# Kernel optimization log

Hardware: AMD Instinct MI355X
Metric: run time of the kernel (lower is better)

Reference implementation:

```python
import jax, jax.numpy as jnp
import numpy as np

NEG_SLOPE = 0.2


def gat_conv(x, src, dst, W, a_src, a_dst, bias, concat, num_nodes):
    # x: [N, F_in]; W: [F_in, H*C]; a_src/a_dst: [H, C]
    H, C = a_src.shape
    h = (x @ W).reshape(num_nodes, H, C)               # [N,H,C]
    alpha_s = jnp.sum(h * a_src[None], axis=-1)        # [N,H]
    alpha_d = jnp.sum(h * a_dst[None], axis=-1)        # [N,H]
    e = jax.nn.leaky_relu(alpha_s[src] + alpha_d[dst], NEG_SLOPE)  # [E,H]
    m = jax.ops.segment_max(e, dst, num_segments=num_nodes)
    m = jnp.where(jnp.isfinite(m), m, 0.0)
    ex = jnp.exp(e - m[dst])
    denom = jax.ops.segment_sum(ex, dst, num_segments=num_nodes)
    alpha = ex / (denom[dst] + 1e-16)                  # scatter-softmax over dst
    msg = h[src] * alpha[:, :, None]                   # [E,H,C]
    out = jax.ops.segment_sum(msg, dst, num_segments=num_nodes)  # [N,H,C]
    if concat:
        out = out.reshape(num_nodes, H * C)
    else:
        out = out.mean(axis=1)
    return out + bias


def setup_inputs() -> dict:
    key = jax.random.key(0)
    ks = jax.random.split(key, 12)
    N, E = 50000, 800000
    num_concat, F_in, hid, H1, H2, n_cls = 2, 128, 64, 4, 1, 16
    x_list = jax.random.normal(ks[0], (num_concat, N, F_in), dtype=jnp.float32)
    edge_index = jax.random.randint(ks[1], (2, E), 0, N, dtype=jnp.int64)
    s = 0.1
    W1 = jax.random.normal(ks[2], (num_concat, F_in, H1 * hid), dtype=jnp.float32) * s
    att_src1 = jax.random.normal(ks[3], (num_concat, H1, hid), dtype=jnp.float32) * s
    att_dst1 = jax.random.normal(ks[4], (num_concat, H1, hid), dtype=jnp.float32) * s
    bias1 = jnp.zeros((num_concat, H1 * hid), dtype=jnp.float32)
    W2 = jax.random.normal(ks[5], (hid * H1 * num_concat, H2 * n_cls), dtype=jnp.float32) * s
    att_src2 = jax.random.normal(ks[6], (H2, n_cls), dtype=jnp.float32) * s
    att_dst2 = jax.random.normal(ks[7], (H2, n_cls), dtype=jnp.float32) * s
    bias2 = jnp.zeros((n_cls,), dtype=jnp.float32)
    return {"x_list": x_list, "edge_index": edge_index,
            "W1": W1, "att_src1": att_src1, "att_dst1": att_dst1, "bias1": bias1,
            "W2": W2, "att_src2": att_src2, "att_dst2": att_dst2, "bias2": bias2}


def reference(x_list, edge_index, W1, att_src1, att_dst1, bias1, W2, att_src2, att_dst2, bias2):
    num_concat, N, _ = x_list.shape
    loop = jnp.arange(N, dtype=edge_index.dtype)
    src = jnp.concatenate([edge_index[0], loop])  # PyG add_self_loops=True
    dst = jnp.concatenate([edge_index[1], loop])
    hidden = [jax.nn.elu(gat_conv(x_list[k], src, dst, W1[k], att_src1[k], att_dst1[k],
                                  bias1[k], True, N))
              for k in range(num_concat)]
    x = jnp.concatenate(hidden, axis=-1)           # [N, hid*H1*num_concat]
    out = gat_conv(x, src, dst, W2, att_src2, att_dst2, bias2, False, N)
    return out
```

## Files before the change

### kernel.cpp

```cpp
#include <hip/hip_runtime.h>

#define LEAKY(v) ((v) >= 0.0f ? (v) : 0.2f * (v))

typedef __attribute__((ext_vector_type(8))) short bf16x8;
typedef __attribute__((ext_vector_type(4))) float f32x4;

__device__ __forceinline__ unsigned short f2bf(float f) {
    unsigned int u = __float_as_uint(f);
    unsigned int r = u + 0x7FFFu + ((u >> 16) & 1u);
    return (unsigned short)(r >> 16);
}
__device__ __forceinline__ unsigned int pk2(float a, float b) {
    return (unsigned int)f2bf(a) | ((unsigned int)f2bf(b) << 16);
}
__device__ __forceinline__ float lo16(unsigned int u) { return __uint_as_float(u << 16); }
__device__ __forceinline__ float hi16(unsigned int u) { return __uint_as_float(u & 0xFFFF0000u); }


__global__ __launch_bounds__(256) void count_deg(const int* ei, int* deg, int E, int Etot) {
    int i = blockIdx.x * 256 + threadIdx.x;
    if (i >= Etot) return;
    int d = (i < E) ? ei[E + i] : (i - E);
    atomicAdd(&deg[d], 1);
}

__global__ __launch_bounds__(512) void scan_block(const int* deg, int* excl, int* bsum, int n) {
    __shared__ int s[512];
    int t = threadIdx.x;
    int i = blockIdx.x * 512 + t;
    int v = (i < n) ? deg[i] : 0;
    s[t] = v;
    __syncthreads();
    for (int d = 1; d < 512; d <<= 1) {
        int x = 0;
        if (t >= d) x = s[t - d];
        __syncthreads();
        if (t >= d) s[t] += x;
        __syncthreads();
    }
    if (i < n) excl[i] = s[t] - v;
    if (t == 511) bsum[blockIdx.x] = s[511];
}

__global__ __launch_bounds__(512) void scan_sums(const int* bsum, int* boff, int nb) {
    __shared__ int s[512];
    int t = threadIdx.x;
    int v = (t < nb) ? bsum[t] : 0;
    s[t] = v;
    __syncthreads();
    for (int d = 1; d < 512; d <<= 1) {
        int x = 0;
        if (t >= d) x = s[t - d];
        __syncthreads();
        if (t >= d) s[t] += x;
        __syncthreads();
    }
    boff[t] = s[t] - v;
}

__global__ __launch_bounds__(256) void finalize_off(int* csr, int* cursor, const int* boff, int n, int etot) {
    int i = blockIdx.x * 256 + threadIdx.x;
    if (i < n) {
        int v = csr[i] + boff[i >> 9];
        csr[i] = v;
        cursor[i] = v;
    }
    if (i == 0) csr[n] = etot;
}

__global__ __launch_bounds__(256) void scatter_edge(const int* ei, int* cursor, int* srcs, int* dsts,
                                                    int E, int Etot) {
    int i = blockIdx.x * 256 + threadIdx.x;
    if (i >= Etot) return;
    int s, d;
    if (i < E) { s = ei[i]; d = ei[E + i]; }
    else       { s = i - E; d = s; }
    int pos = atomicAdd(&cursor[d], 1);
    srcs[pos] = s;
    dsts[pos] = d;
}


__global__ __launch_bounds__(256) void wpack(const float* __restrict__ W1, unsigned short* __restrict__ wt1,
                                             const float* __restrict__ W2, unsigned short* __restrict__ wt2) {
    int id = blockIdx.x * 256 + threadIdx.x;
    if (id < 8192) {
        int conv = id >> 12, rem = id & 4095;
        int c = rem >> 4, q = rem & 15;
        const float* src = W1 + (size_t)conv * 32768 + (size_t)(q * 8) * 256 + c;
        float w[8];
#pragma unroll
        for (int j = 0; j < 8; ++j) w[j] = src[j * 256];
        uint4 v;
        v.x = pk2(w[0], w[1]); v.y = pk2(w[2], w[3]);
        v.z = pk2(w[4], w[5]); v.w = pk2(w[6], w[7]);
        *(uint4*)(wt1 + (size_t)conv * 32768 + c * 128 + ((q ^ (c & 7)) << 3)) = v;
    } else if (id < 9216) {
        int id2 = id - 8192;
        int s = id2 >> 6, l = id2 & 63;
        const float* src = W2 + (size_t)(s * 32 + (l >> 4) * 8) * 16 + (l & 15);
        float w[8];
#pragma unroll
        for (int j = 0; j < 8; ++j) w[j] = src[j * 16];
        uint4 v;
        v.x = pk2(w[0], w[1]); v.y = pk2(w[2], w[3]);
        v.z = pk2(w[4], w[5]); v.w = pk2(w[6], w[7]);
        *(uint4*)(wt2 + (size_t)id2 * 8) = v;
    }
}


__global__ __launch_bounds__(256) void gemm1_mfma(const float* __restrict__ x_list,
                                                  const unsigned short* __restrict__ wt1,
                                                  const float* __restrict__ asw, const float* __restrict__ adw,
                                                  unsigned short* __restrict__ hp,
                                                  float* __restrict__ aad, int N) {
    __shared__ unsigned short As[64 * 128];
    __shared__ unsigned short Ws[256 * 128];
    int conv = blockIdx.y;
    int t = threadIdx.x;
    int w = t >> 6, l = t & 63;

    const float* xg = x_list + (size_t)conv * N * 128;
#pragma unroll
    for (int p = 0; p < 4; ++p) {
        int id = p * 256 + t;
        int row = id >> 4, q = id & 15;
        int grow = blockIdx.x * 64 + row;
        uint4 v = make_uint4(0, 0, 0, 0);
        if (grow < N) {
            const float* src = xg + (size_t)grow * 128 + q * 8;
            float4 a = *(const float4*)src;
            float4 b = *(const float4*)(src + 4);
            v.x = pk2(a.x, a.y); v.y = pk2(a.z, a.w);
            v.z = pk2(b.x, b.y); v.w = pk2(b.z, b.w);
        }
        *(uint4*)(As + row * 128 + ((q ^ (row & 7)) << 3)) = v;
    }
    const uint4* wsrc = (const uint4*)(wt1 + (size_t)conv * 32768);
#pragma unroll
    for (int p = 0; p < 16; ++p) {
        int id = p * 256 + t;
        *(uint4*)(Ws + (size_t)id * 8) = wsrc[id];
    }
    __syncthreads();

    f32x4 acc[4][4];
#pragma unroll
    for (int mt = 0; mt < 4; ++mt)
#pragma unroll
        for (int nt = 0; nt < 4; ++nt) acc[mt][nt] = (f32x4){0.f, 0.f, 0.f, 0.f};

    int lr = l & 15, lg = l >> 4;
#pragma unroll
    for (int s = 0; s < 4; ++s) {
        int kq = s * 4 + lg;
        bf16x8 af[4], bf[4];
#pragma unroll
        for (int mt = 0; mt < 4; ++mt) {
            int r = mt * 16 + lr;
            af[mt] = *(const bf16x8*)(As + r * 128 + ((kq ^ (r & 7)) << 3));
        }
#pragma unroll
        for (int nt = 0; nt < 4; ++nt) {
            int c = w * 64 + nt * 16 + lr;
            bf[nt] = *(const bf16x8*)(Ws + c * 128 + ((kq ^ (c & 7)) << 3));
        }
#pragma unroll
        for (int mt = 0; mt < 4; ++mt)
#pragma unroll
            for (int nt = 0; nt < 4; ++nt)
                acc[mt][nt] = __builtin_amdgcn_mfma_f32_16x16x32_bf16(bf[nt], af[mt], acc[mt][nt], 0, 0, 0);
    }

    float4 aswv[4], adwv[4];
#pragma unroll
    for (int nt = 0; nt < 4; ++nt) {
        aswv[nt] = *(const float4*)(asw + conv * 256 + w * 64 + nt * 16 + lg * 4);
        adwv[nt] = *(const float4*)(adw + conv * 256 + w * 64 + nt * 16 + lg * 4);
    }
#pragma unroll
    for (int mt = 0; mt < 4; ++mt) {
        int grow = blockIdx.x * 64 + mt * 16 + lr;
        bool ok = grow < N;
        float sv = 0.f, dv = 0.f;
#pragma unroll
        for (int nt = 0; nt < 4; ++nt) {
            f32x4 a = acc[mt][nt];
            if (ok) {
                uint2 pk;
                pk.x = pk2(a[0], a[1]);
                pk.y = pk2(a[2], a[3]);
                *(uint2*)(hp + (size_t)grow * 512 + conv * 256 + w * 64 + nt * 16 + lg * 4) = pk;
            }
            sv += a[0] * aswv[nt].x + a[1] * aswv[nt].y + a[2] * aswv[nt].z + a[3] * aswv[nt].w;
            dv += a[0] * adwv[nt].x + a[1] * adwv[nt].y + a[2] * adwv[nt].z + a[3] * adwv[nt].w;
        }
        sv += __shfl_xor(sv, 16); sv += __shfl_xor(sv, 32);
        dv += __shfl_xor(dv, 16); dv += __shfl_xor(dv, 32);
        if (l < 16 && ok) {
            aad[(size_t)grow * 16 + conv * 4 + w]     = sv;
            aad[(size_t)grow * 16 + 8 + conv * 4 + w] = dv;
        }
    }
}


__global__ __launch_bounds__(256) void edge_w1(const int* __restrict__ srcs, const int* __restrict__ dsts,
                                               const float* __restrict__ aad,
                                               float* __restrict__ pw, int Etot) {
    int e = blockIdx.x * 256 + threadIdx.x;
    if (e >= Etot) return;
    int s = srcs[e], d = dsts[e];
    float4 as_lo = *(const float4*)(aad + (size_t)s * 16);
    float4 as_hi = *(const float4*)(aad + (size_t)s * 16 + 4);
    float4 ad_lo = *(const float4*)(aad + (size_t)d * 16 + 8);
    float4 ad_hi = *(const float4*)(aad + (size_t)d * 16 + 12);
    float4 p0, p1;
    p0.x = __expf(LEAKY(as_lo.x + ad_lo.x));
    p0.y = __expf(LEAKY(as_lo.y + ad_lo.y));
    p0.z = __expf(LEAKY(as_lo.z + ad_lo.z));
    p0.w = __expf(LEAKY(as_lo.w + ad_lo.w));
    p1.x = __expf(LEAKY(as_hi.x + ad_hi.x));
    p1.y = __expf(LEAKY(as_hi.y + ad_hi.y));
    p1.z = __expf(LEAKY(as_hi.z + ad_hi.z));
    p1.w = __expf(LEAKY(as_hi.w + ad_hi.w));
    *(float4*)(pw + (size_t)e * 8)     = p0;
    *(float4*)(pw + (size_t)e * 8 + 4) = p1;
}


__global__ __launch_bounds__(256) void agg1_both(const unsigned short* __restrict__ hp,
                                                 const float* __restrict__ pw,
                                                 const int* __restrict__ off, const int* __restrict__ srcs,
                                                 const float* __restrict__ b1,
                                                 unsigned short* __restrict__ x2, int N) {
    int n = blockIdx.x * 4 + (threadIdx.x >> 6);
    int lane = threadIdx.x & 63;
    if (n >= N) return;
    int r0 = off[n], r1 = off[n + 1];
    int ch = lane >> 3;

    float acc[8] = {0.f, 0.f, 0.f, 0.f, 0.f, 0.f, 0.f, 0.f};
    float den = 0.f;

    for (int base = r0; base < r1; base += 64) {
        int cnt = min(64, r1 - base);
        int my = (base + lane < r1) ? srcs[base + lane] : 0;
        int j = 0;
        for (; j + 2 <= cnt; j += 2) {
            int s0 = __shfl(my, j);
            int s1 = __shfl(my, j + 1);
            uint4 g0 = *(const uint4*)(hp + (size_t)s0 * 512 + lane * 8);
            uint4 g1 = *(const uint4*)(hp + (size_t)s1 * 512 + lane * 8);
            float p0 = pw[(size_t)(base + j) * 8 + ch];
            float p1 = pw[(size_t)(base + j + 1) * 8 + ch];
            den += p0; den += p1;
            acc[0] += p0 * lo16(g0.x); acc[1] += p0 * hi16(g0.x);
            acc[2] += p0 * lo16(g0.y); acc[3] += p0 * hi16(g0.y);
            acc[4] += p0 * lo16(g0.z); acc[5] += p0 * hi16(g0.z);
            acc[6] += p0 * lo16(g0.w); acc[7] += p0 * hi16(g0.w);
            acc[0] += p1 * lo16(g1.x); acc[1] += p1 * hi16(g1.x);
            acc[2] += p1 * lo16(g1.y); acc[3] += p1 * hi16(g1.y);
            acc[4] += p1 * lo16(g1.z); acc[5] += p1 * hi16(g1.z);
            acc[6] += p1 * lo16(g1.w); acc[7] += p1 * hi16(g1.w);
        }
        if (j < cnt) {
            int s0 = __shfl(my, j);
            uint4 g0 = *(const uint4*)(hp + (size_t)s0 * 512 + lane * 8);
            float p0 = pw[(size_t)(base + j) * 8 + ch];
            den += p0;
            acc[0] += p0 * lo16(g0.x); acc[1] += p0 * hi16(g0.x);
            acc[2] += p0 * lo16(g0.y); acc[3] += p0 * hi16(g0.y);
            acc[4] += p0 * lo16(g0.z); acc[5] += p0 * hi16(g0.z);
            acc[6] += p0 * lo16(g0.w); acc[7] += p0 * hi16(g0.w);
        }
    }

    float inv = 1.f / (den + 1e-16f);
    const float* bp = b1 + lane * 8;
    unsigned int ow[4];
#pragma unroll
    for (int q = 0; q < 4; ++q) {
        float o0 = acc[q * 2 + 0] * inv + bp[q * 2 + 0];
        float o1 = acc[q * 2 + 1] * inv + bp[q * 2 + 1];
        o0 = o0 > 0.f ? o0 : (__expf(o0) - 1.0f);
        o1 = o1 > 0.f ? o1 : (__expf(o1) - 1.0f);
        ow[q] = pk2(o0, o1);
    }
    uint4 ov = make_uint4(ow[0], ow[1], ow[2], ow[3]);
    *(uint4*)(x2 + (size_t)n * 512 + lane * 8) = ov;
}


__global__ __launch_bounds__(256) void gemm2_mfma(const unsigned short* __restrict__ x2,
                                                  const unsigned short* __restrict__ wt2,
                                                  const float* __restrict__ asw2, const float* __restrict__ adw2,
                                                  float* __restrict__ h2,
                                                  float* __restrict__ as2, float* __restrict__ ad2, int N) {
    int t = threadIdx.x;
    int w = t >> 6, l = t & 63;
    int rowbase = (blockIdx.x * 4 + w) * 16;
    if (rowbase >= N) return;
    int lr = l & 15, lg = l >> 4;

    f32x4 acc = (f32x4){0.f, 0.f, 0.f, 0.f};
    const unsigned short* ap = x2 + (size_t)(rowbase + lr) * 512 + lg * 8;
#pragma unroll
    for (int s = 0; s < 16; ++s) {
        bf16x8 av = *(const bf16x8*)(ap + s * 32);
        bf16x8 bv = *(const bf16x8*)(wt2 + ((size_t)s * 64 + l) * 8);
        acc = __builtin_amdgcn_mfma_f32_16x16x32_bf16(av, bv, acc, 0, 0, 0);
    }

    float asv = asw2[lr], adv = adw2[lr];
#pragma unroll
    for (int i = 0; i < 4; ++i) {
        int row = rowbase + lg * 4 + i;
        if (row < N) h2[(size_t)row * 16 + lr] = acc[i];
        float sv = acc[i] * asv, dv = acc[i] * adv;
#pragma unroll
        for (int o = 1; o < 16; o <<= 1) {
            sv += __shfl_xor(sv, o);
            dv += __shfl_xor(dv, o);
        }
        if (lr == 0 && row < N) { as2[row] = sv; ad2[row] = dv; }
    }
}


__global__ __launch_bounds__(256) void agg2(const float* __restrict__ h2,
                                            const float* __restrict__ as2, const float* __restrict__ ad2,
                                            const int* __restrict__ off, const int* __restrict__ srcs,
                                            const float* __restrict__ bias2, float* __restrict__ out, int N) {
    int n = blockIdx.x * 4 + (threadIdx.x >> 6);
    int lane = threadIdx.x & 63;
    if (n >= N) return;
    int r0 = off[n], r1 = off[n + 1];
    float adn = ad2[n];
    int cg = lane & 3, eo = lane >> 2;

    float4 acc = make_float4(0.f, 0.f, 0.f, 0.f);
    float den = 0.f;
    for (int base = r0; base + eo < r1; base += 16) {
        int e = base + eo;
        int s = srcs[e];
        float p = __expf(LEAKY(as2[s] + adn));
        float4 hv = *(const float4*)(h2 + (size_t)s * 16 + cg * 4);
        den += p;
        acc.x += p * hv.x; acc.y += p * hv.y;
        acc.z += p * hv.z; acc.w += p * hv.w;
    }
#pragma unroll
    for (int o = 4; o < 64; o <<= 1) {
        acc.x += __shfl_xor(acc.x, o);
        acc.y += __shfl_xor(acc.y, o);
        acc.z += __shfl_xor(acc.z, o);
        acc.w += __shfl_xor(acc.w, o);
        den   += __shfl_xor(den, o);
    }
    if (eo == 0) {
        float inv = 1.f / (den + 1e-16f);
        float4 b = *(const float4*)(bias2 + cg * 4);
        float4 o4;
        o4.x = acc.x * inv + b.x;
        o4.y = acc.y * inv + b.y;
        o4.z = acc.z * inv + b.z;
        o4.w = acc.w * inv + b.w;
        *(float4*)(out + (size_t)n * 16 + cg * 4) = o4;
    }
}


extern "C" void kernel_launch(void* const* d_in, const int* in_sizes, int n_in,
                              void* d_out, int out_size, void* d_ws, size_t ws_size,
                              hipStream_t stream) {
    const float* x_list = (const float*)d_in[0];
    const int*   ei     = (const int*)d_in[1];
    const float* W1     = (const float*)d_in[2];
    const float* as1w   = (const float*)d_in[3];
    const float* ad1w   = (const float*)d_in[4];
    const float* b1     = (const float*)d_in[5];
    const float* W2     = (const float*)d_in[6];
    const float* as2w   = (const float*)d_in[7];
    const float* ad2w   = (const float*)d_in[8];
    const float* b2     = (const float*)d_in[9];
    float* out = (float*)d_out;

    const int N = in_sizes[0] / 256;
    const int E = in_sizes[1] / 2;
    const int Etot = E + N;

    char* ws = (char*)d_ws;
    size_t woff = 0;
    auto alloc = [&](size_t bytes) {
        char* p = ws + woff;
        woff = (woff + bytes + 255) & ~(size_t)255;
        return p;
    };
    int*   csr    = (int*)alloc((size_t)(N + 1) * 4);
    int*   cursor = (int*)alloc((size_t)N * 4);
    int*   srcs   = (int*)alloc((size_t)Etot * 4);
    int*   dsts   = (int*)alloc((size_t)Etot * 4);
    int*   bsum   = (int*)alloc(512 * 4);
    int*   boff   = (int*)alloc(512 * 4);
    float* aad    = (float*)alloc((size_t)N * 16 * 4);
    float* as2    = (float*)alloc((size_t)N * 4);
    float* ad2    = (float*)alloc((size_t)N * 4);
    unsigned short* wt1 = (unsigned short*)alloc(2 * 32768 * 2);
    unsigned short* wt2 = (unsigned short*)alloc(16 * 64 * 8 * 2);
    unsigned short* hp  = (unsigned short*)alloc((size_t)N * 512 * 2);
    unsigned short* x2  = (unsigned short*)alloc((size_t)N * 512 * 2);
    float* h2     = (float*)alloc((size_t)N * 16 * 4);
    float* pw     = (float*)alloc((size_t)Etot * 8 * 4);

    hipMemsetAsync(cursor, 0, (size_t)N * 4, stream);
    int gE = (Etot + 255) / 256;
    count_deg<<<gE, 256, 0, stream>>>(ei, cursor, E, Etot);
    int nb = (N + 511) / 512;
    scan_block<<<nb, 512, 0, stream>>>(cursor, csr, bsum, N);
    scan_sums<<<1, 512, 0, stream>>>(bsum, boff, nb);
    finalize_off<<<(N + 255) / 256, 256, 0, stream>>>(csr, cursor, boff, N, Etot);
    scatter_edge<<<gE, 256, 0, stream>>>(ei, cursor, srcs, dsts, E, Etot);

    wpack<<<36, 256, 0, stream>>>(W1, wt1, W2, wt2);

    gemm1_mfma<<<dim3((N + 63) / 64, 2), 256, 0, stream>>>(x_list, wt1, as1w, ad1w, hp, aad, N);
    edge_w1<<<gE, 256, 0, stream>>>(srcs, dsts, aad, pw, Etot);
    agg1_both<<<(N + 3) / 4, 256, 0, stream>>>(hp, pw, csr, srcs, b1, x2, N);

    gemm2_mfma<<<(N + 63) / 64, 256, 0, stream>>>(x2, wt2, as2w, ad2w, h2, as2, ad2, N);
    agg2<<<(N + 3) / 4, 256, 0, stream>>>(h2, as2, ad2, csr, srcs, b2, out, N);
}
```

Before: 308.5 us.

## Fuse second-layer GEMM and attention logits into layer-1 aggregation epilogue

The layer-1 aggregation kernel now multiplies each node's ELU output directly by W2 (fp32, per-lane partial dot products plus a wavefront butterfly reduction) and writes h2, as2 and ad2, removing the bf16 x2 intermediate and the separate MFMA gemm2 kernel. This avoids writing and re-reading about 51 MB of x2 and one kernel launch. The trade is 128 extra FMAs per lane and a 16-value, 6-step shuffle reduction per node, which adds latency and register pressure to an already gather-bound kernel. Precision also changes, since layer-2 input is no longer rounded to bf16.

Result: slower. 436.7 us (+41.6%).

```diff
diff --git a/kernel.cpp b/kernel.cpp
--- a/kernel.cpp
+++ b/kernel.cpp
@@ -81,32 +81,19 @@
 }
 
 
-__global__ __launch_bounds__(256) void wpack(const float* __restrict__ W1, unsigned short* __restrict__ wt1,
-                                             const float* __restrict__ W2, unsigned short* __restrict__ wt2) {
+__global__ __launch_bounds__(256) void wpack(const float* __restrict__ W1, unsigned short* __restrict__ wt1) {
     int id = blockIdx.x * 256 + threadIdx.x;
-    if (id < 8192) {
-        int conv = id >> 12, rem = id & 4095;
-        int c = rem >> 4, q = rem & 15;
-        const float* src = W1 + (size_t)conv * 32768 + (size_t)(q * 8) * 256 + c;
-        float w[8];
-#pragma unroll
-        for (int j = 0; j < 8; ++j) w[j] = src[j * 256];
-        uint4 v;
-        v.x = pk2(w[0], w[1]); v.y = pk2(w[2], w[3]);
-        v.z = pk2(w[4], w[5]); v.w = pk2(w[6], w[7]);
-        *(uint4*)(wt1 + (size_t)conv * 32768 + c * 128 + ((q ^ (c & 7)) << 3)) = v;
-    } else if (id < 9216) {
-        int id2 = id - 8192;
-        int s = id2 >> 6, l = id2 & 63;
-        const float* src = W2 + (size_t)(s * 32 + (l >> 4) * 8) * 16 + (l & 15);
-        float w[8];
-#pragma unroll
-        for (int j = 0; j < 8; ++j) w[j] = src[j * 16];
-        uint4 v;
-        v.x = pk2(w[0], w[1]); v.y = pk2(w[2], w[3]);
-        v.z = pk2(w[4], w[5]); v.w = pk2(w[6], w[7]);
-        *(uint4*)(wt2 + (size_t)id2 * 8) = v;
-    }
+    if (id >= 8192) return;
+    int conv = id >> 12, rem = id & 4095;
+    int c = rem >> 4, q = rem & 15;
+    const float* src = W1 + (size_t)conv * 32768 + (size_t)(q * 8) * 256 + c;
+    float w[8];
+#pragma unroll
+    for (int j = 0; j < 8; ++j) w[j] = src[j * 256];
+    uint4 v;
+    v.x = pk2(w[0], w[1]); v.y = pk2(w[2], w[3]);
+    v.z = pk2(w[4], w[5]); v.w = pk2(w[6], w[7]);
+    *(uint4*)(wt1 + (size_t)conv * 32768 + c * 128 + ((q ^ (c & 7)) << 3)) = v;
 }
 
 
@@ -230,11 +217,14 @@
 }
 
 
-__global__ __launch_bounds__(256) void agg1_both(const unsigned short* __restrict__ hp,
-                                                 const float* __restrict__ pw,
-                                                 const int* __restrict__ off, const int* __restrict__ srcs,
-                                                 const float* __restrict__ b1,
-                                                 unsigned short* __restrict__ x2, int N) {
+__global__ __launch_bounds__(256) void agg1_fused(const unsigned short* __restrict__ hp,
+                                                  const float* __restrict__ pw,
+                                                  const int* __restrict__ off, const int* __restrict__ srcs,
+                                                  const float* __restrict__ b1,
+                                                  const float* __restrict__ W2,
+                                                  const float* __restrict__ asw2, const float* __restrict__ adw2,
+                                                  float* __restrict__ h2,
+                                                  float* __restrict__ as2, float* __restrict__ ad2, int N) {
     int n = blockIdx.x * 4 + (threadIdx.x >> 6);
     int lane = threadIdx.x & 63;
     if (n >= N) return;
@@ -279,52 +269,59 @@
 
     float inv = 1.f / (den + 1e-16f);
     const float* bp = b1 + lane * 8;
-    unsigned int ow[4];
-#pragma unroll
-    for (int q = 0; q < 4; ++q) {
-        float o0 = acc[q * 2 + 0] * inv + bp[q * 2 + 0];
-        float o1 = acc[q * 2 + 1] * inv + bp[q * 2 + 1];
-        o0 = o0 > 0.f ? o0 : (__expf(o0) - 1.0f);
-        o1 = o1 > 0.f ? o1 : (__expf(o1) - 1.0f);
-        ow[q] = pk2(o0, o1);
-    }
-    uint4 ov = make_uint4(ow[0], ow[1], ow[2], ow[3]);
-    *(uint4*)(x2 + (size_t)n * 512 + lane * 8) = ov;
-}
-
-
-__global__ __launch_bounds__(256) void gemm2_mfma(const unsigned short* __restrict__ x2,
-                                                  const unsigned short* __restrict__ wt2,
-                                                  const float* __restrict__ asw2, const float* __restrict__ adw2,
-                                                  float* __restrict__ h2,
-                                                  float* __restrict__ as2, float* __restrict__ ad2, int N) {
-    int t = threadIdx.x;
-    int w = t >> 6, l = t & 63;
-    int rowbase = (blockIdx.x * 4 + w) * 16;
-    if (rowbase >= N) return;
-    int lr = l & 15, lg = l >> 4;
-
-    f32x4 acc = (f32x4){0.f, 0.f, 0.f, 0.f};
-    const unsigned short* ap = x2 + (size_t)(rowbase + lr) * 512 + lg * 8;
-#pragma unroll
-    for (int s = 0; s < 16; ++s) {
-        bf16x8 av = *(const bf16x8*)(ap + s * 32);
-        bf16x8 bv = *(const bf16x8*)(wt2 + ((size_t)s * 64 + l) * 8);
-        acc = __builtin_amdgcn_mfma_f32_16x16x32_bf16(av, bv, acc, 0, 0, 0);
-    }
-
-    float asv = asw2[lr], adv = adw2[lr];
-#pragma unroll
-    for (int i = 0; i < 4; ++i) {
-        int row = rowbase + lg * 4 + i;
-        if (row < N) h2[(size_t)row * 16 + lr] = acc[i];
-        float sv = acc[i] * asv, dv = acc[i] * adv;
-#pragma unroll
-        for (int o = 1; o < 16; o <<= 1) {
-            sv += __shfl_xor(sv, o);
-            dv += __shfl_xor(dv, o);
-        }
-        if (lr == 0 && row < N) { as2[row] = sv; ad2[row] = dv; }
+#pragma unroll
+    for (int q = 0; q < 8; ++q) {
+        float o = acc[q] * inv + bp[q];
+        acc[q] = o > 0.f ? o : (__expf(o) - 1.0f);
+    }
+
+    float part[16];
+#pragma unroll
+    for (int c = 0; c < 16; ++c) part[c] = 0.f;
+    const float* w2p = W2 + (size_t)lane * 128;
+#pragma unroll
+    for (int q = 0; q < 8; ++q) {
+        float x = acc[q];
+        const float* wr = w2p + q * 16;
+#pragma unroll
+        for (int c4 = 0; c4 < 4; ++c4) {
+            float4 wv = *(const float4*)(wr + c4 * 4);
+            part[c4 * 4 + 0] += x * wv.x;
+            part[c4 * 4 + 1] += x * wv.y;
+            part[c4 * 4 + 2] += x * wv.z;
+            part[c4 * 4 + 3] += x * wv.w;
+        }
+    }
+#pragma unroll
+    for (int o = 1; o < 64; o <<= 1) {
+#pragma unroll
+        for (int c = 0; c < 16; ++c) part[c] += __shfl_xor(part[c], o);
+    }
+
+    if (lane == 0) {
+        float4 a2lo = *(const float4*)(asw2);
+        float4 a2hi = *(const float4*)(asw2 + 4);
+        float4 a2l2 = *(const float4*)(asw2 + 8);
+        float4 a2h2 = *(const float4*)(asw2 + 12);
+        float4 d2lo = *(const float4*)(adw2);
+        float4 d2hi = *(const float4*)(adw2 + 4);
+        float4 d2l2 = *(const float4*)(adw2 + 8);
+        float4 d2h2 = *(const float4*)(adw2 + 12);
+        float sv = part[0] * a2lo.x + part[1] * a2lo.y + part[2] * a2lo.z + part[3] * a2lo.w
+                 + part[4] * a2hi.x + part[5] * a2hi.y + part[6] * a2hi.z + part[7] * a2hi.w
+                 + part[8] * a2l2.x + part[9] * a2l2.y + part[10] * a2l2.z + part[11] * a2l2.w
+                 + part[12] * a2h2.x + part[13] * a2h2.y + part[14] * a2h2.z + part[15] * a2h2.w;
+        float dv = part[0] * d2lo.x + part[1] * d2lo.y + part[2] * d2lo.z + part[3] * d2lo.w
+                 + part[4] * d2hi.x + part[5] * d2hi.y + part[6] * d2hi.z + part[7] * d2hi.w
+                 + part[8] * d2l2.x + part[9] * d2l2.y + part[10] * d2l2.z + part[11] * d2l2.w
+                 + part[12] * d2h2.x + part[13] * d2h2.y + part[14] * d2h2.z + part[15] * d2h2.w;
+        float* ho = h2 + (size_t)n * 16;
+        *(float4*)(ho)      = make_float4(part[0], part[1], part[2], part[3]);
+        *(float4*)(ho + 4)  = make_float4(part[4], part[5], part[6], part[7]);
+        *(float4*)(ho + 8)  = make_float4(part[8], part[9], part[10], part[11]);
+        *(float4*)(ho + 12) = make_float4(part[12], part[13], part[14], part[15]);
+        as2[n] = sv;
+        ad2[n] = dv;
     }
 }
 
@@ -408,9 +405,7 @@
     float* as2    = (float*)alloc((size_t)N * 4);
     float* ad2    = (float*)alloc((size_t)N * 4);
     unsigned short* wt1 = (unsigned short*)alloc(2 * 32768 * 2);
-    unsigned short* wt2 = (unsigned short*)alloc(16 * 64 * 8 * 2);
     unsigned short* hp  = (unsigned short*)alloc((size_t)N * 512 * 2);
-    unsigned short* x2  = (unsigned short*)alloc((size_t)N * 512 * 2);
     float* h2     = (float*)alloc((size_t)N * 16 * 4);
     float* pw     = (float*)alloc((size_t)Etot * 8 * 4);
 
@@ -423,12 +418,12 @@
     finalize_off<<<(N + 255) / 256, 256, 0, stream>>>(csr, cursor, boff, N, Etot);
     scatter_edge<<<gE, 256, 0, stream>>>(ei, cursor, srcs, dsts, E, Etot);
 
-    wpack<<<36, 256, 0, stream>>>(W1, wt1, W2, wt2);
+    wpack<<<32, 256, 0, stream>>>(W1, wt1);
 
     gemm1_mfma<<<dim3((N + 63) / 64, 2), 256, 0, stream>>>(x_list, wt1, as1w, ad1w, hp, aad, N);
     edge_w1<<<gE, 256, 0, stream>>>(srcs, dsts, aad, pw, Etot);
-    agg1_both<<<(N + 3) / 4, 256, 0, stream>>>(hp, pw, csr, srcs, b1, x2, N);
-
-    gemm2_mfma<<<(N + 63) / 64, 256, 0, stream>>>(x2, wt2, as2w, ad2w, h2, as2, ad2, N);
+    agg1_fused<<<(N + 3) / 4, 256, 0, stream>>>(hp, pw, csr, srcs, b1, W2, as2w, ad2w,
+                                                h2, as2, ad2, N);
+
     agg2<<<(N + 3) / 4, 256, 0, stream>>>(h2, as2, ad2, csr, srcs, b2, out, N);
 }
```
